# Optimization experiments

Measured on AMD Instinct MI355X. Metric: run time of the kernel, lower is better.

The kernel has to match this reference:

```python
import jax, jax.numpy as jnp
import numpy as np

# graph sizes (DGL block convention: dst nodes are a prefix of src nodes)
N0, N1, N2, N3 = 200000, 150000, 120000, 100000
E0, E1, E2, ESUB = 2_000_000, 1_000_000, 500_000, 250_000
NUM_RELS, REL_DIM = 500, 32
H1, H2, OUT_DIM = 256, 256, 256


def setup_inputs() -> dict:
    key = jax.random.key(0)
    ks = jax.random.split(key, 24)
    ri = lambda k, n, hi: jax.random.randint(k, (n,), 0, hi, dtype=jnp.int32)
    rn = lambda k, shp, s=0.05: (jax.random.normal(k, shp, dtype=jnp.float32) * s)
    return {
        # block0 (edge-type aggregation): src in [0,N0), dst in [0,N1)
        'e0_type': ri(ks[0], E0, NUM_RELS),
        'e0_src': ri(ks[1], E0, N0),
        'e0_dst': ri(ks[2], E0, N1),
        # block1: src in [0,N1), dst in [0,N2)
        'e1_src': ri(ks[3], E1, N1),
        'e1_dst': ri(ks[4], E1, N2),
        # block2: src in [0,N2), dst in [0,N3)
        'e2_src': ri(ks[5], E2, N2),
        'e2_dst': ri(ks[6], E2, N3),
        # edge_subg over final N3 nodes
        'sub_src': ri(ks[7], ESUB, N3),
        'sub_dst': ri(ks[8], ESUB, N3),
        # learned params
        'rel_emb': rn(ks[9], (NUM_RELS, REL_DIM), 1.0),
        'W_out': rn(ks[10], (REL_DIM, REL_DIM)), 'b_out': rn(ks[11], (REL_DIM,)),
        'W_in': rn(ks[12], (REL_DIM, REL_DIM)), 'b_in': rn(ks[13], (REL_DIM,)),
        'W1': rn(ks[14], (2 * REL_DIM, H1)), 'b1': rn(ks[15], (H1,)),
        'W2': rn(ks[16], (H1, H2)), 'b2': rn(ks[17], (H2,)),
        'Wfc': rn(ks[18], (2 * H2, OUT_DIM)), 'bfc': rn(ks[19], (OUT_DIM,)),
    }


def _mean_agg(edge_feat, idx, num_nodes):
    # sparse incidence mm followed by div(degree): per-node mean of incident edge feats
    s = jax.ops.segment_sum(edge_feat, idx, num_segments=num_nodes)
    deg = jax.ops.segment_sum(jnp.ones((edge_feat.shape[0],), edge_feat.dtype), idx,
                              num_segments=num_nodes)
    return s / jnp.maximum(deg, 1.0)[:, None]


def _graph_conv(x, src, dst, n_src, n_dst, W, b):
    # DGL GraphConv, norm='both', degrees clamped to min 1
    ones_e = jnp.ones((src.shape[0],), x.dtype)
    deg_o = jax.ops.segment_sum(ones_e, src, num_segments=n_src)
    deg_i = jax.ops.segment_sum(ones_e, dst, num_segments=n_dst)
    h = x * jax.lax.rsqrt(jnp.maximum(deg_o, 1.0))[:, None]
    agg = jax.ops.segment_sum(h[src], dst, num_segments=n_dst)
    agg = agg * jax.lax.rsqrt(jnp.maximum(deg_i, 1.0))[:, None]
    return agg @ W + b


def reference(e0_type, e0_src, e0_dst, e1_src, e1_dst, e2_src, e2_dst,
              sub_src, sub_dst, rel_emb, W_out, b_out, W_in, b_in,
              W1, b1, W2, b2, Wfc, bfc):
    emb = rel_emb[e0_type]                                  # [E0, 32]
    out_agg = _mean_agg(emb @ W_out + b_out, e0_src, N0)    # [N0, 32]
    in_agg = _mean_agg(emb @ W_in + b_in, e0_dst, N1)       # [N1, 32]
    in_agg = jnp.pad(in_agg, ((0, N0 - N1), (0, 0)))        # pad to input_nodes
    x = jnp.concatenate([out_agg, in_agg], axis=1)          # [N0, 64]
    x = x[:N1]                                              # Identical: block0 dst feats
    x = jax.nn.relu(_graph_conv(x, e1_src, e1_dst, N1, N2, W1, b1))  # [N2, H1]
    x = jax.nn.relu(_graph_conv(x, e2_src, e2_dst, N2, N3, W2, b2))  # [N3, H2]
    edge_emb = jnp.concatenate([x[sub_src], x[sub_dst]], axis=1)     # [ESUB, 2*H2]
    return edge_emb @ Wfc + bfc                                      # [ESUB, OUT_DIM]
```

## Files before the change

kernel.cpp:

```cpp
#include <hip/hip_runtime.h>
#include <hip/hip_bf16.h>

#define N0 200000
#define N1 150000
#define N2 120000
#define N3 100000
#define E0 2000000
#define E1 1000000
#define E2 500000
#define ESUB 250000

#define IC2 0
#define IC1 N3
#define I0S (N3 + N2)
#define I0D (N3 + N2 + N1)
#define LALL (N3 + N2 + 2 * N1)

#define NC2  ((N3 + 511) / 512)
#define NC1  ((N2 + 511) / 512)
#define NC0B ((N1 + 511) / 512)
#define CB2  0
#define CB1  NC2
#define CB0S (NC2 + NC1)
#define CB0D (NC2 + NC1 + NC0B)
#define NBALL (NC2 + NC1 + 2 * NC0B)

#define BINCHUNK 4096
#define POOLCAP (E2 + E1 + 2 * E0)

typedef float f32x4 __attribute__((ext_vector_type(4)));
typedef __bf16 bf16x8 __attribute__((ext_vector_type(8)));

__global__ __launch_bounds__(256) void k_cntb0(const int* __restrict__ src, const int* __restrict__ dst,
                                               int* __restrict__ bcnt) {
    __shared__ int lcnt[1024];
    int t = threadIdx.x;
#pragma unroll
    for (int j = 0; j < 4; j++) lcnt[t + j * 256] = 0;
    __syncthreads();
    int e0 = blockIdx.x * BINCHUNK;
    int e1 = E0 - e0; if (e1 > BINCHUNK) e1 = BINCHUNK; e1 += e0;
    for (int i = e0 + t; i < e1; i += 256) {
        int s = src[i];
        if (s < N1) atomicAdd(&lcnt[s >> 9], 1);
        atomicAdd(&lcnt[512 + (dst[i] >> 9)], 1);
    }
    __syncthreads();
    for (int b = t; b < 1024; b += 256) {
        int c = lcnt[b];
        if (c > 0) atomicAdd(&bcnt[(b >= 512 ? CB0D - 512 : CB0S) + b], c);
    }
}

__global__ __launch_bounds__(256) void k_cnt2b(const int* __restrict__ src, const int* __restrict__ dst,
                                               int n, int* __restrict__ dego,
                                               int* __restrict__ bcnt, int bbase) {
    __shared__ int lcnt[512];
    int t = threadIdx.x;
    lcnt[t] = 0; lcnt[t + 256] = 0;
    __syncthreads();
    int e0 = blockIdx.x * BINCHUNK;
    int e1 = n - e0; if (e1 > BINCHUNK) e1 = BINCHUNK; e1 += e0;
    for (int i = e0 + t; i < e1; i += 256) {
        atomicAdd(&dego[src[i]], 1);
        atomicAdd(&lcnt[dst[i] >> 9], 1);
    }
    __syncthreads();
    for (int b = t; b < 512; b += 256) {
        int c = lcnt[b];
        if (c > 0) atomicAdd(&bcnt[bbase + b], c);
    }
}

__global__ __launch_bounds__(256) void k_bscanA(const int* __restrict__ bcnt, int* __restrict__ boffs) {
    __shared__ int A[1024], B[1024];
    int t = threadIdx.x;
    for (int i = t; i < 1024; i += 256) A[i] = (i < NBALL) ? bcnt[i] : 0;
    __syncthreads();
    int* cur = A; int* nxt = B;
    for (int off = 1; off < 1024; off <<= 1) {
        for (int i = t; i < 1024; i += 256) nxt[i] = cur[i] + (i >= off ? cur[i - off] : 0);
        __syncthreads();
        int* tmp = cur; cur = nxt; nxt = tmp;
    }
    for (int i = t; i < NBALL; i += 256) boffs[i + 1] = cur[i];
    if (t == 0) boffs[0] = 0;
}

__global__ __launch_bounds__(256) void k_binA(const int* __restrict__ dst, const int* __restrict__ aux,
                                              int n, const int* __restrict__ boffs,
                                              int* __restrict__ bcur, int ccbase,
                                              int* __restrict__ cpool) {
    __shared__ int lcnt[512], lbase[512], lcur[512];
    int t = threadIdx.x;
    lcnt[t] = 0; lcnt[t + 256] = 0;
    lcur[t] = 0; lcur[t + 256] = 0;
    __syncthreads();
    int e0 = blockIdx.x * BINCHUNK;
    int e1 = n - e0; if (e1 > BINCHUNK) e1 = BINCHUNK; e1 += e0;
    for (int i = e0 + t; i < e1; i += 256) {
        atomicAdd(&lcnt[dst[i] >> 9], 1);
    }
    __syncthreads();
    for (int b = t; b < 512; b += 256) {
        int c = lcnt[b];
        if (c > 0) lbase[b] = boffs[ccbase + b] + atomicAdd(&bcur[ccbase + b], c);
    }
    __syncthreads();
    for (int i = e0 + t; i < e1; i += 256) {
        int d = dst[i];
        int b = d >> 9;
        int r = atomicAdd(&lcur[b], 1);
        cpool[lbase[b] + r] = ((d & 511) << 18) | aux[i];
    }
}

__global__ __launch_bounds__(256) void k_binA0b(const int* __restrict__ typ,
                                                const int* __restrict__ src, const int* __restrict__ dst,
                                                const int* __restrict__ boffs,
                                                int* __restrict__ bcur, int* __restrict__ cpool) {
    __shared__ int lcnt[1024], lbase[1024], lcur[1024];
    int t = threadIdx.x;
#pragma unroll
    for (int j = 0; j < 4; j++) { lcnt[t + j * 256] = 0; lcur[t + j * 256] = 0; }
    __syncthreads();
    int e0 = blockIdx.x * BINCHUNK;
    int e1 = E0 - e0; if (e1 > BINCHUNK) e1 = BINCHUNK; e1 += e0;
    for (int i = e0 + t; i < e1; i += 256) {
        int s = src[i];
        if (s < N1) atomicAdd(&lcnt[s >> 9], 1);
        atomicAdd(&lcnt[512 + (dst[i] >> 9)], 1);
    }
    __syncthreads();
    for (int b = t; b < 1024; b += 256) {
        int c = lcnt[b];
        if (c > 0) {
            int idx = (b >= 512 ? CB0D - 512 : CB0S) + b;
            lbase[b] = boffs[idx] + atomicAdd(&bcur[idx], c);
        }
    }
    __syncthreads();
    for (int i = e0 + t; i < e1; i += 256) {
        int ty = typ[i];
        int s = src[i];
        if (s < N1) {
            int b = s >> 9;
            int r = atomicAdd(&lcur[b], 1);
            cpool[lbase[b] + r] = ((s & 511) << 18) | ty;
        }
        int d = dst[i];
        int b2 = 512 + (d >> 9);
        int r2 = atomicAdd(&lcur[b2], 1);
        cpool[lbase[b2] + r2] = ((d & 511) << 18) | ty;
    }
}

__global__ __launch_bounds__(256) void k_binBall(const int* __restrict__ boffs,
                                                 const int* __restrict__ cpool,
                                                 int* __restrict__ pool,
                                                 int* __restrict__ cntN, int* __restrict__ offsN) {
    __shared__ int lcnt[512], lexc[512];
    int t = threadIdx.x;
    int g = blockIdx.x;
    int cbase, n0, nseg;
    if (g < CB1)       { cbase = IC2; n0 = g << 9;            nseg = N3; }
    else if (g < CB0S) { cbase = IC1; n0 = (g - CB1) << 9;    nseg = N2; }
    else if (g < CB0D) { cbase = I0S; n0 = (g - CB0S) << 9;   nseg = N1; }
    else               { cbase = I0D; n0 = (g - CB0D) << 9;   nseg = N1; }
    int nodes = nseg - n0; if (nodes > 512) nodes = 512;
    lcnt[t] = 0; lcnt[t + 256] = 0;
    __syncthreads();
    int R0 = boffs[g], R1 = boffs[g + 1];
    for (int i = R0 + t; i < R1; i += 256) atomicAdd(&lcnt[cpool[i] >> 18], 1);
    __syncthreads();
    lexc[t] = lcnt[t]; lexc[t + 256] = lcnt[t + 256];
    __syncthreads();
    for (int off = 1; off < 512; off <<= 1) {
        int a0 = (t >= off) ? lexc[t - off] : 0;
        int a1 = (t + 256 >= off) ? lexc[t + 256 - off] : 0;
        __syncthreads();
        lexc[t] += a0; lexc[t + 256] += a1;
        __syncthreads();
    }
#pragma unroll
    for (int jj = 0; jj < 2; jj++) {
        int j = t + jj * 256;
        int c = lcnt[j];
        int ex = lexc[j] - c;
        if (j < nodes) { cntN[cbase + n0 + j] = c; offsN[cbase + n0 + j] = R0 + ex; }
        lexc[j] = ex; lcnt[j] = 0;
    }
    __syncthreads();
    for (int i = R0 + t; i < R1; i += 256) {
        int p = cpool[i];
        int low = p >> 18;
        int r = atomicAdd(&lcnt[low], 1);
        pool[R0 + lexc[low] + r] = p & 0x3FFFF;
    }
}

__global__ __launch_bounds__(256) void k_layer0(const int* __restrict__ cntN, const int* __restrict__ offsN,
                                                const int* __restrict__ pool, const float* __restrict__ rel_emb,
                                                const float* __restrict__ W_out, const float* __restrict__ b_out,
                                                const float* __restrict__ W_in, const float* __restrict__ b_in,
                                                const int* __restrict__ deg1o, float* __restrict__ h1) {
    __shared__ float S[4][64];
    int t = threadIdx.x;
    int nl = t >> 6;
    int lane = t & 63;
    int half = lane >> 5;
    int k = lane & 31;
    int n = blockIdx.x * 4 + nl;
    int ci = (half ? I0D : I0S) + n;
    int dg = cntN[ci];
    int off = offsN[ci];
    float acc = 0.0f;
    for (int cb = 0; cb < dg; cb += 32) {
        int rem = dg - cb; if (rem > 32) rem = 32;
        int ty_all = (k < rem) ? pool[off + cb + k] : 0;
        int i2 = 0;
        for (; i2 + 4 <= rem; i2 += 4) {
            int t0 = __shfl(ty_all, i2,     32);
            int t1 = __shfl(ty_all, i2 + 1, 32);
            int t2 = __shfl(ty_all, i2 + 2, 32);
            int t3 = __shfl(ty_all, i2 + 3, 32);
            float a0 = rel_emb[t0 * 32 + k];
            float a1 = rel_emb[t1 * 32 + k];
            float a2 = rel_emb[t2 * 32 + k];
            float a3 = rel_emb[t3 * 32 + k];
            acc += a0; acc += a1; acc += a2; acc += a3;
        }
        for (; i2 < rem; i2++) {
            int ty = __shfl(ty_all, i2, 32);
            acc += rel_emb[ty * 32 + k];
        }
    }
    S[nl][lane] = (dg > 0) ? acc / (float)dg : 0.0f;
    __syncthreads();
    const float* W = half ? W_in : W_out;
    float b = half ? b_in[k] : b_out[k];
    float r = 0.0f;
    if (dg > 0) {
        float d = 0.0f;
#pragma unroll
        for (int kk = 0; kk < 32; kk++) d += S[nl][half * 32 + kk] * W[kk * 32 + k];
        r = d + b;
    }
    h1[(size_t)n * 64 + lane] = r * rsqrtf(fmaxf((float)deg1o[n], 1.0f));
}

__global__ __launch_bounds__(256) void k_conv1g(const float* __restrict__ h1,
                                                const int* __restrict__ cntN, const int* __restrict__ offsN,
                                                const int* __restrict__ pool, const int* __restrict__ deg2o,
                                                const float* __restrict__ W1, const float* __restrict__ b1,
                                                __bf16* __restrict__ h2b) {
    __shared__ float row[8][64];
    int base = blockIdx.x * 8;
    int t = threadIdx.x;
    int wave = t >> 6, lane = t & 63;
#pragma unroll
    for (int rr = 0; rr < 2; rr++) {
        int m = wave * 2 + rr;
        int rg = base + m;
        int dg = cntN[IC1 + rg];
        int off = offsN[IC1 + rg];
        float acc = 0.0f;
        for (int cb = 0; cb < dg; cb += 64) {
            int rem = dg - cb; if (rem > 64) rem = 64;
            int s_all = (lane < rem) ? pool[off + cb + lane] : 0;
            int i = 0;
            for (; i + 4 <= rem; i += 4) {
                int s0 = __shfl(s_all, i,     64);
                int s1 = __shfl(s_all, i + 1, 64);
                int s2 = __shfl(s_all, i + 2, 64);
                int s3 = __shfl(s_all, i + 3, 64);
                float a0 = h1[(size_t)s0 * 64 + lane];
                float a1 = h1[(size_t)s1 * 64 + lane];
                float a2 = h1[(size_t)s2 * 64 + lane];
                float a3 = h1[(size_t)s3 * 64 + lane];
                acc += a0; acc += a1; acc += a2; acc += a3;
            }
            for (; i < rem; i++) {
                int s = __shfl(s_all, i, 64);
                acc += h1[(size_t)s * 64 + lane];
            }
        }
        row[m][lane] = acc * rsqrtf(fmaxf((float)dg, 1.0f));
    }
    __syncthreads();
    float acc8[8] = {0, 0, 0, 0, 0, 0, 0, 0};
    for (int k = 0; k < 64; k++) {
        float w = W1[k * 256 + t];
#pragma unroll
        for (int m = 0; m < 8; m++) acc8[m] += row[m][k] * w;
    }
    float bb = b1[t];
#pragma unroll
    for (int m = 0; m < 8; m++) {
        float v = fmaxf(acc8[m] + bb, 0.0f) * rsqrtf(fmaxf((float)deg2o[base + m], 1.0f));
        h2b[(size_t)(base + m) * 256 + t] = (__bf16)v;
    }
}

__global__ void k_pack(const float* __restrict__ W, __bf16* __restrict__ Wp, int ksteps) {
    int idx = blockIdx.x * 256 + threadIdx.x;
    int j = idx & 7;
    int lane = (idx >> 3) & 63;
    int rest = idx >> 9;
    int ks = rest % ksteps;
    int tn = rest / ksteps;
    int k = ks * 32 + ((lane >> 4) * 8) + j;
    int n = tn * 16 + (lane & 15);
    Wp[idx] = (__bf16)W[k * 256 + n];
}

__global__ __launch_bounds__(256) void k_conv2g(const __bf16* __restrict__ h2b,
                                                const int* __restrict__ cntN, const int* __restrict__ offsN,
                                                const int* __restrict__ pool,
                                                const __bf16* __restrict__ W2p,
                                                const float* __restrict__ b2v,
                                                __bf16* __restrict__ x3b) {
    __shared__ __bf16 At[64][264];
    int t = threadIdx.x;
    int base = blockIdx.x * 64;
    int wave = t >> 6, lane = t & 63;
#pragma unroll 1
    for (int rr = 0; rr < 16; rr++) {
        int row = wave * 16 + rr;
        int rg = base + row;
        float a0 = 0.f, a1 = 0.f, a2 = 0.f, a3 = 0.f;
        int dg = 0;
        if (rg < N3) {
            dg = cntN[IC2 + rg];
            int off = offsN[IC2 + rg];
            for (int cb = 0; cb < dg; cb += 64) {
                int rem = dg - cb; if (rem > 64) rem = 64;
                int s_all = (lane < rem) ? pool[off + cb + lane] : 0;
                int i = 0;
                for (; i + 4 <= rem; i += 4) {
                    int s0 = __shfl(s_all, i,     64);
                    int s1 = __shfl(s_all, i + 1, 64);
                    int s2 = __shfl(s_all, i + 2, 64);
                    int s3 = __shfl(s_all, i + 3, 64);
                    union { ushort4 u; __bf16 b[4]; } v0, v1, v2, v3;
                    v0.u = *(const ushort4*)(h2b + (size_t)s0 * 256 + lane * 4);
                    v1.u = *(const ushort4*)(h2b + (size_t)s1 * 256 + lane * 4);
                    v2.u = *(const ushort4*)(h2b + (size_t)s2 * 256 + lane * 4);
                    v3.u = *(const ushort4*)(h2b + (size_t)s3 * 256 + lane * 4);
                    a0 += ((float)v0.b[0] + (float)v1.b[0]) + ((float)v2.b[0] + (float)v3.b[0]);
                    a1 += ((float)v0.b[1] + (float)v1.b[1]) + ((float)v2.b[1] + (float)v3.b[1]);
                    a2 += ((float)v0.b[2] + (float)v1.b[2]) + ((float)v2.b[2] + (float)v3.b[2]);
                    a3 += ((float)v0.b[3] + (float)v1.b[3]) + ((float)v2.b[3] + (float)v3.b[3]);
                }
                for (; i < rem; i++) {
                    int s0 = __shfl(s_all, i, 64);
                    union { ushort4 u; __bf16 b[4]; } v0;
                    v0.u = *(const ushort4*)(h2b + (size_t)s0 * 256 + lane * 4);
                    a0 += (float)v0.b[0]; a1 += (float)v0.b[1];
                    a2 += (float)v0.b[2]; a3 += (float)v0.b[3];
                }
            }
        }
        float sc = rsqrtf(fmaxf((float)dg, 1.0f));
        union { __bf16 b[4]; uint2 u; } cv;
        cv.b[0] = (__bf16)(a0 * sc); cv.b[1] = (__bf16)(a1 * sc);
        cv.b[2] = (__bf16)(a2 * sc); cv.b[3] = (__bf16)(a3 * sc);
        *(uint2*)&At[row][lane * 4] = cv.u;
    }
    __syncthreads();
    int q = lane >> 4, r16 = lane & 15;
    f32x4 acc[4][4] = {};
    for (int ks = 0; ks < 8; ks++) {
        bf16x8 a[4], b[4];
        int ko = ks * 32 + q * 8;
#pragma unroll
        for (int mt = 0; mt < 4; mt++)
            a[mt] = *(const bf16x8*)&At[mt * 16 + r16][ko];
#pragma unroll
        for (int i = 0; i < 4; i++) {
            int tn = wave * 4 + i;
            b[i] = *(const bf16x8*)&W2p[((size_t)(tn * 8 + ks) * 64 + lane) * 8];
        }
#pragma unroll
        for (int mt = 0; mt < 4; mt++)
#pragma unroll
            for (int i = 0; i < 4; i++)
                acc[mt][i] = __builtin_amdgcn_mfma_f32_16x16x32_bf16(a[mt], b[i], acc[mt][i], 0, 0, 0);
    }
#pragma unroll
    for (int mt = 0; mt < 4; mt++) {
#pragma unroll
        for (int i = 0; i < 4; i++) {
            int col = (wave * 4 + i) * 16 + r16;
            float bb = b2v[col];
#pragma unroll
            for (int rr = 0; rr < 4; rr++) {
                int row = base + mt * 16 + q * 4 + rr;
                if (row < N3)
                    x3b[(size_t)row * 256 + col] = (__bf16)fmaxf(acc[mt][i][rr] + bb, 0.0f);
            }
        }
    }
}

__global__ __launch_bounds__(256) void k_final_mfma(const int* __restrict__ ss, const int* __restrict__ sd,
                                                    const __bf16* __restrict__ x3b,
                                                    const __bf16* __restrict__ Wp,
                                                    const float* __restrict__ bfc,
                                                    float* __restrict__ out) {
    __shared__ __bf16 At[64][520];
    __shared__ int eidx[128];
    int t = threadIdx.x;
    int base = blockIdx.x * 64;
    if (t < 64)       { int e = base + t;      eidx[t] = ss[e < ESUB ? e : ESUB - 1]; }
    else if (t < 128) { int e = base + t - 64; eidx[t] = sd[e < ESUB ? e : ESUB - 1]; }
    __syncthreads();
#pragma unroll
    for (int it = 0; it < 16; it++) {
        int c = it * 256 + t;
        int row = c >> 6;
        int cpos = c & 63;
        int half = cpos >> 5;
        int off8 = (cpos & 31) * 8;
        int node = eidx[half * 64 + row];
        uint4 v = *(const uint4*)(x3b + (size_t)node * 256 + off8);
        *(uint4*)&At[row][half * 256 + off8] = v;
    }
    __syncthreads();
    int wave = t >> 6, lane = t & 63;
    int q = lane >> 4, r16 = lane & 15;
    f32x4 acc[4][4] = {};
    for (int ks = 0; ks < 16; ks++) {
        bf16x8 a[4], b[4];
        int ko = ks * 32 + q * 8;
#pragma unroll
        for (int mt = 0; mt < 4; mt++)
            a[mt] = *(const bf16x8*)&At[mt * 16 + r16][ko];
#pragma unroll
        for (int i = 0; i < 4; i++) {
            int tn = wave * 4 + i;
            b[i] = *(const bf16x8*)&Wp[((size_t)(tn * 16 + ks) * 64 + lane) * 8];
        }
#pragma unroll
        for (int mt = 0; mt < 4; mt++)
#pragma unroll
            for (int i = 0; i < 4; i++)
                acc[mt][i] = __builtin_amdgcn_mfma_f32_16x16x32_bf16(a[mt], b[i], acc[mt][i], 0, 0, 0);
    }
#pragma unroll
    for (int mt = 0; mt < 4; mt++) {
#pragma unroll
        for (int i = 0; i < 4; i++) {
            int col = (wave * 4 + i) * 16 + r16;
            float bb = bfc[col];
#pragma unroll
            for (int rr = 0; rr < 4; rr++) {
                int row = base + mt * 16 + q * 4 + rr;
                if (row < ESUB)
                    out[(size_t)row * 256 + col] = acc[mt][i][rr] + bb;
            }
        }
    }
}

extern "C" void kernel_launch(void* const* d_in, const int* in_sizes, int n_in,
                              void* d_out, int out_size, void* d_ws, size_t ws_size,
                              hipStream_t stream) {
    const int* e0_type = (const int*)d_in[0];
    const int* e0_src  = (const int*)d_in[1];
    const int* e0_dst  = (const int*)d_in[2];
    const int* e1_src  = (const int*)d_in[3];
    const int* e1_dst  = (const int*)d_in[4];
    const int* e2_src  = (const int*)d_in[5];
    const int* e2_dst  = (const int*)d_in[6];
    const int* sub_src = (const int*)d_in[7];
    const int* sub_dst = (const int*)d_in[8];
    const float* rel_emb = (const float*)d_in[9];
    const float* W_out   = (const float*)d_in[10];
    const float* b_out   = (const float*)d_in[11];
    const float* W_in    = (const float*)d_in[12];
    const float* b_in    = (const float*)d_in[13];
    const float* W1      = (const float*)d_in[14];
    const float* b1      = (const float*)d_in[15];
    const float* W2      = (const float*)d_in[16];
    const float* b2v     = (const float*)d_in[17];
    const float* Wfc     = (const float*)d_in[18];
    const float* bfc     = (const float*)d_in[19];
    float* out = (float*)d_out;

    int* bcnt  = (int*)d_ws;
    int* bcur  = bcnt + 1024;
    int* deg1o = bcur + 1024;
    int* deg2o = deg1o + N1;
    int* boffs = deg2o + N2;
    int* cntN  = boffs + 1025;
    int* offsN = cntN + LALL;
    int* pool  = offsN + LALL;
    int* cpool = pool + POOLCAP;
    float* h1  = (float*)(cpool + POOLCAP);
    __bf16* h2b = (__bf16*)(h1 + (size_t)N1 * 64);
    __bf16* Wfcp = (__bf16*)(h2b + (size_t)N2 * 256);
    __bf16* W2p  = Wfcp + 131072;
    __bf16* x3b  = (__bf16*)(pool + E2);

    const int BT = 256;

    hipMemsetAsync(d_ws, 0, (size_t)(1024 + 1024 + N1 + N2) * sizeof(int), stream);

    k_pack<<<512, BT, 0, stream>>>(Wfc, Wfcp, 16);
    k_pack<<<256, BT, 0, stream>>>(W2, W2p, 8);

    int nbA0 = (E0 + BINCHUNK - 1) / BINCHUNK;
    int nbA1 = (E1 + BINCHUNK - 1) / BINCHUNK;
    int nbA2 = (E2 + BINCHUNK - 1) / BINCHUNK;
    k_cntb0<<<nbA0, BT, 0, stream>>>(e0_src, e0_dst, bcnt);
    k_cnt2b<<<nbA1, BT, 0, stream>>>(e1_src, e1_dst, E1, deg1o, bcnt, CB1);
    k_cnt2b<<<nbA2, BT, 0, stream>>>(e2_src, e2_dst, E2, deg2o, bcnt, CB2);

    k_bscanA<<<1, BT, 0, stream>>>(bcnt, boffs);

    k_binA<<<nbA2, BT, 0, stream>>>(e2_dst, e2_src, E2, boffs, bcur, CB2, cpool);
    k_binA0b<<<nbA0, BT, 0, stream>>>(e0_type, e0_src, e0_dst, boffs, bcur, cpool);
    k_binA<<<nbA1, BT, 0, stream>>>(e1_dst, e1_src, E1, boffs, bcur, CB1, cpool);

    k_binBall<<<NBALL, BT, 0, stream>>>(boffs, cpool, pool, cntN, offsN);

    k_layer0<<<N1 / 4, BT, 0, stream>>>(cntN, offsN, pool, rel_emb, W_out, b_out, W_in, b_in, deg1o, h1);

    k_conv1g<<<N2 / 8, BT, 0, stream>>>(h1, cntN, offsN, pool, deg2o, W1, b1, h2b);

    k_conv2g<<<(N3 + 63) / 64, BT, 0, stream>>>(h2b, cntN, offsN, pool, W2p, b2v, x3b);

    k_final_mfma<<<(ESUB + 63) / 64, BT, 0, stream>>>(sub_src, sub_dst, x3b, Wfcp, bfc, out);
}
```

Baseline: 980.0 us.

## Precompute relation-embedding projections and store layer-0 features in bf16

A new small kernel precomputes rel_emb@W_out and rel_emb@W_in for all 500 relation types. Layer 0 then gathers these projected rows directly and only adds the bias, which removes the per-node 32x32 matvec and the shared-memory sync. The h1 features are now stored in bf16, and conv1 gathers two bf16 per lane across half-waves, processing two edges per wave step. This halves gather traffic at the cost of bf16 rounding on the intermediate features.

```diff
diff --git a/kernel.cpp b/kernel.cpp
--- a/kernel.cpp
+++ b/kernel.cpp
@@ -31,6 +31,22 @@
 typedef float f32x4 __attribute__((ext_vector_type(4)));
 typedef __bf16 bf16x8 __attribute__((ext_vector_type(8)));
 
+__global__ __launch_bounds__(256) void k_rew(const float* __restrict__ rel_emb,
+                                             const float* __restrict__ W_out,
+                                             const float* __restrict__ W_in,
+                                             float* __restrict__ REW) {
+    int idx = blockIdx.x * 256 + threadIdx.x;
+    if (idx >= 32000) return;
+    int side = idx / 16000;
+    int rest = idx - side * 16000;
+    int ty = rest >> 5, k = rest & 31;
+    const float* W = side ? W_in : W_out;
+    float s = 0.f;
+#pragma unroll
+    for (int j = 0; j < 32; j++) s += rel_emb[ty * 32 + j] * W[j * 32 + k];
+    REW[idx] = s;
+}
+
 __global__ __launch_bounds__(256) void k_cntb0(const int* __restrict__ src, const int* __restrict__ dst,
                                                int* __restrict__ bcnt) {
     __shared__ int lcnt[1024];
@@ -199,12 +215,10 @@
     }
 }
 
-__global__ __launch_bounds__(256) void k_layer0(const int* __restrict__ cntN, const int* __restrict__ offsN,
-                                                const int* __restrict__ pool, const float* __restrict__ rel_emb,
-                                                const float* __restrict__ W_out, const float* __restrict__ b_out,
-                                                const float* __restrict__ W_in, const float* __restrict__ b_in,
-                                                const int* __restrict__ deg1o, float* __restrict__ h1) {
-    __shared__ float S[4][64];
+__global__ __launch_bounds__(256) void k_layer0r(const int* __restrict__ cntN, const int* __restrict__ offsN,
+                                                 const int* __restrict__ pool, const float* __restrict__ REW,
+                                                 const float* __restrict__ b_out, const float* __restrict__ b_in,
+                                                 const int* __restrict__ deg1o, __bf16* __restrict__ h1b) {
     int t = threadIdx.x;
     int nl = t >> 6;
     int lane = t & 63;
@@ -214,6 +228,7 @@
     int ci = (half ? I0D : I0S) + n;
     int dg = cntN[ci];
     int off = offsN[ci];
+    const float* R = REW + half * 16000;
     float acc = 0.0f;
     for (int cb = 0; cb < dg; cb += 32) {
         int rem = dg - cb; if (rem > 32) rem = 32;
@@ -224,32 +239,23 @@
             int t1 = __shfl(ty_all, i2 + 1, 32);
             int t2 = __shfl(ty_all, i2 + 2, 32);
             int t3 = __shfl(ty_all, i2 + 3, 32);
-            float a0 = rel_emb[t0 * 32 + k];
-            float a1 = rel_emb[t1 * 32 + k];
-            float a2 = rel_emb[t2 * 32 + k];
-            float a3 = rel_emb[t3 * 32 + k];
+            float a0 = R[t0 * 32 + k];
+            float a1 = R[t1 * 32 + k];
+            float a2 = R[t2 * 32 + k];
+            float a3 = R[t3 * 32 + k];
             acc += a0; acc += a1; acc += a2; acc += a3;
         }
         for (; i2 < rem; i2++) {
             int ty = __shfl(ty_all, i2, 32);
-            acc += rel_emb[ty * 32 + k];
-        }
-    }
-    S[nl][lane] = (dg > 0) ? acc / (float)dg : 0.0f;
-    __syncthreads();
-    const float* W = half ? W_in : W_out;
+            acc += R[ty * 32 + k];
+        }
+    }
     float b = half ? b_in[k] : b_out[k];
-    float r = 0.0f;
-    if (dg > 0) {
-        float d = 0.0f;
-#pragma unroll
-        for (int kk = 0; kk < 32; kk++) d += S[nl][half * 32 + kk] * W[kk * 32 + k];
-        r = d + b;
-    }
-    h1[(size_t)n * 64 + lane] = r * rsqrtf(fmaxf((float)deg1o[n], 1.0f));
-}
-
-__global__ __launch_bounds__(256) void k_conv1g(const float* __restrict__ h1,
+    float r = (dg > 0) ? (acc / (float)dg + b) : 0.0f;
+    h1b[(size_t)n * 64 + lane] = (__bf16)(r * rsqrtf(fmaxf((float)deg1o[n], 1.0f)));
+}
+
+__global__ __launch_bounds__(256) void k_conv1g(const __bf16* __restrict__ h1b,
                                                 const int* __restrict__ cntN, const int* __restrict__ offsN,
                                                 const int* __restrict__ pool, const int* __restrict__ deg2o,
                                                 const float* __restrict__ W1, const float* __restrict__ b1,
@@ -258,34 +264,47 @@
     int base = blockIdx.x * 8;
     int t = threadIdx.x;
     int wave = t >> 6, lane = t & 63;
+    int eo = lane >> 5;
+    int c = lane & 31;
 #pragma unroll
     for (int rr = 0; rr < 2; rr++) {
         int m = wave * 2 + rr;
         int rg = base + m;
         int dg = cntN[IC1 + rg];
         int off = offsN[IC1 + rg];
-        float acc = 0.0f;
+        float a0 = 0.f, a1 = 0.f;
         for (int cb = 0; cb < dg; cb += 64) {
             int rem = dg - cb; if (rem > 64) rem = 64;
             int s_all = (lane < rem) ? pool[off + cb + lane] : 0;
             int i = 0;
-            for (; i + 4 <= rem; i += 4) {
-                int s0 = __shfl(s_all, i,     64);
-                int s1 = __shfl(s_all, i + 1, 64);
-                int s2 = __shfl(s_all, i + 2, 64);
-                int s3 = __shfl(s_all, i + 3, 64);
-                float a0 = h1[(size_t)s0 * 64 + lane];
-                float a1 = h1[(size_t)s1 * 64 + lane];
-                float a2 = h1[(size_t)s2 * 64 + lane];
-                float a3 = h1[(size_t)s3 * 64 + lane];
-                acc += a0; acc += a1; acc += a2; acc += a3;
+            for (; i + 8 <= rem; i += 8) {
+                int sA = __shfl(s_all, i     + eo, 64);
+                int sB = __shfl(s_all, i + 2 + eo, 64);
+                int sC = __shfl(s_all, i + 4 + eo, 64);
+                int sD = __shfl(s_all, i + 6 + eo, 64);
+                union { unsigned u; __bf16 b[2]; } vA, vB, vC, vD;
+                vA.u = *(const unsigned*)(h1b + (size_t)sA * 64 + c * 2);
+                vB.u = *(const unsigned*)(h1b + (size_t)sB * 64 + c * 2);
+                vC.u = *(const unsigned*)(h1b + (size_t)sC * 64 + c * 2);
+                vD.u = *(const unsigned*)(h1b + (size_t)sD * 64 + c * 2);
+                a0 += ((float)vA.b[0] + (float)vB.b[0]) + ((float)vC.b[0] + (float)vD.b[0]);
+                a1 += ((float)vA.b[1] + (float)vB.b[1]) + ((float)vC.b[1] + (float)vD.b[1]);
             }
-            for (; i < rem; i++) {
-                int s = __shfl(s_all, i, 64);
-                acc += h1[(size_t)s * 64 + lane];
+            for (; i < rem; i += 2) {
+                int have = rem - i;
+                int s = __shfl(s_all, i + ((eo < have) ? eo : 0), 64);
+                union { unsigned u; __bf16 b[2]; } v;
+                v.u = *(const unsigned*)(h1b + (size_t)s * 64 + c * 2);
+                if (eo < have) { a0 += (float)v.b[0]; a1 += (float)v.b[1]; }
             }
         }
-        row[m][lane] = acc * rsqrtf(fmaxf((float)dg, 1.0f));
+        a0 += __shfl_xor(a0, 32, 64);
+        a1 += __shfl_xor(a1, 32, 64);
+        if (eo == 0) {
+            float sc = rsqrtf(fmaxf((float)dg, 1.0f));
+            row[m][c * 2]     = a0 * sc;
+            row[m][c * 2 + 1] = a1 * sc;
+        }
     }
     __syncthreads();
     float acc8[8] = {0, 0, 0, 0, 0, 0, 0, 0};
@@ -495,11 +514,12 @@
     int* boffs = deg2o + N2;
     int* cntN  = boffs + 1025;
     int* offsN = cntN + LALL;
-    int* pool  = offsN + LALL;
+    float* REW = (float*)(offsN + LALL);
+    int* pool  = (int*)(REW + 32000);
     int* cpool = pool + POOLCAP;
-    float* h1  = (float*)(cpool + POOLCAP);
-    __bf16* h2b = (__bf16*)(h1 + (size_t)N1 * 64);
-    __bf16* Wfcp = (__bf16*)(h2b + (size_t)N2 * 256);
+    __bf16* h1b = (__bf16*)(cpool + POOLCAP);
+    __bf16* h2b = h1b + (size_t)N1 * 64;
+    __bf16* Wfcp = h2b + (size_t)N2 * 256;
     __bf16* W2p  = Wfcp + 131072;
     __bf16* x3b  = (__bf16*)(pool + E2);
 
@@ -509,6 +529,7 @@
 
     k_pack<<<512, BT, 0, stream>>>(Wfc, Wfcp, 16);
     k_pack<<<256, BT, 0, stream>>>(W2, W2p, 8);
+    k_rew<<<125, BT, 0, stream>>>(rel_emb, W_out, W_in, REW);
 
     int nbA0 = (E0 + BINCHUNK - 1) / BINCHUNK;
     int nbA1 = (E1 + BINCHUNK - 1) / BINCHUNK;
@@ -525,9 +546,9 @@
 
     k_binBall<<<NBALL, BT, 0, stream>>>(boffs, cpool, pool, cntN, offsN);
 
-    k_layer0<<<N1 / 4, BT, 0, stream>>>(cntN, offsN, pool, rel_emb, W_out, b_out, W_in, b_in, deg1o, h1);
-
-    k_conv1g<<<N2 / 8, BT, 0, stream>>>(h1, cntN, offsN, pool, deg2o, W1, b1, h2b);
+    k_layer0r<<<N1 / 4, BT, 0, stream>>>(cntN, offsN, pool, REW, b_out, b_in, deg1o, h1b);
+
+    k_conv1g<<<N2 / 8, BT, 0, stream>>>(h1b, cntN, offsN, pool, deg2o, W1, b1, h2b);
 
     k_conv2g<<<(N3 + 63) / 64, BT, 0, stream>>>(h2b, cntN, offsN, pool, W2p, b2v, x3b);
 
```

Result: faster. 954.9 us (-2.6%).
